# Kernel optimization log

Measured on AMD Instinct MI355X. Metric: run time of the kernel, lower is better.

## Reference

```python
import jax, jax.numpy as jnp
import numpy as np

D_MODEL = 1024
H = 16
D_K = D_MODEL // H
D_FF = 4096
EPS = 1e-6


def setup_inputs() -> dict:
    key = jax.random.key(0)
    ks = jax.random.split(key, 16)
    s = 1.0 / np.sqrt(D_MODEL)
    sf = 1.0 / np.sqrt(D_FF)
    inp = {
        'x': jax.random.normal(ks[0], (4, 2048, D_MODEL), dtype=jnp.float32),
        'wq': jax.random.uniform(ks[1], (D_MODEL, D_MODEL), minval=-s, maxval=s),
        'bq': jax.random.uniform(ks[2], (D_MODEL,), minval=-s, maxval=s),
        'wk': jax.random.uniform(ks[3], (D_MODEL, D_MODEL), minval=-s, maxval=s),
        'bk': jax.random.uniform(ks[4], (D_MODEL,), minval=-s, maxval=s),
        'wv': jax.random.uniform(ks[5], (D_MODEL, D_MODEL), minval=-s, maxval=s),
        'bv': jax.random.uniform(ks[6], (D_MODEL,), minval=-s, maxval=s),
        'wo': jax.random.uniform(ks[7], (D_MODEL, D_MODEL), minval=-s, maxval=s),
        'bo': jax.random.uniform(ks[8], (D_MODEL,), minval=-s, maxval=s),
        'w1': jax.random.uniform(ks[9], (D_MODEL, D_FF), minval=-s, maxval=s),
        'b1': jax.random.uniform(ks[10], (D_FF,), minval=-s, maxval=s),
        'w2': jax.random.uniform(ks[11], (D_FF, D_MODEL), minval=-sf, maxval=sf),
        'b2': jax.random.uniform(ks[12], (D_MODEL,), minval=-sf, maxval=sf),
        'alpha1': jnp.ones((1,), jnp.float32),
        'bias1': jnp.zeros((1,), jnp.float32),
        'alpha2': jnp.ones((1,), jnp.float32),
        'bias2': jnp.zeros((1,), jnp.float32),
    }
    return inp


def _layer_norm(x, alpha, bias):
    # torch: alpha*(x-mean)/(std+eps)+bias with unbiased std (ddof=1), eps on std
    m = jnp.mean(x, axis=-1, keepdims=True)
    s = jnp.std(x, axis=-1, keepdims=True, ddof=1)
    return alpha * (x - m) / (s + EPS) + bias


def _mha(x, wq, bq, wk, bk, wv, bv, wo, bo):
    B, S, _ = x.shape
    q = (x @ wq + bq).reshape(B, S, H, D_K).transpose(0, 2, 1, 3)
    k = (x @ wk + bk).reshape(B, S, H, D_K).transpose(0, 2, 1, 3)
    v = (x @ wv + bv).reshape(B, S, H, D_K).transpose(0, 2, 1, 3)
    scores = jnp.einsum('bhqd,bhkd->bhqk', q, k) / np.sqrt(D_K)
    attn = jax.nn.softmax(scores, axis=-1)
    out = jnp.einsum('bhqk,bhkd->bhqd', attn, v)
    out = out.transpose(0, 2, 1, 3).reshape(B, S, D_MODEL)
    return out @ wo + bo


def reference(x, wq, bq, wk, bk, wv, bv, wo, bo, w1, b1, w2, b2,
              alpha1, bias1, alpha2, bias2):
    # Residual 1: x + MHA(LN(x))
    h = x + _mha(_layer_norm(x, alpha1, bias1), wq, bq, wk, bk, wv, bv, wo, bo)
    # Residual 2: h + FFN(LN(h)); FFN = W2 relu(W1 z + b1) + b2
    z = _layer_norm(h, alpha2, bias2)
    ffn = jax.nn.relu(z @ w1 + b1) @ w2 + b2
    return h + ffn
```

## Files before the change

kernel.cpp:

```cpp
#include <hip/hip_runtime.h>
#include <hip/hip_bf16.h>
#include <cstdint>
#include <cstddef>

typedef __bf16 bf16;
typedef __bf16 bf16x4 __attribute__((ext_vector_type(4)));
typedef __bf16 bf16x8 __attribute__((ext_vector_type(8)));
typedef float f32x4 __attribute__((ext_vector_type(4)));

#define QK_SCALE 0.1803368801111204f

#define AS1 __attribute__((address_space(1)))
#define AS3 __attribute__((address_space(3)))

__device__ __forceinline__ void gload_lds16(const void* g, void* l) {
  __builtin_amdgcn_global_load_lds((AS1 void*)g, (AS3 void*)l, 16, 0, 0);
}

__device__ __forceinline__ float b2f(unsigned short u) {
  union { unsigned int i; float f; } v; v.i = (unsigned int)u << 16; return v.f;
}

__global__ __launch_bounds__(256)
void transpose_cvt(const float* __restrict__ in, bf16* __restrict__ out,
                   int K, int N) {
  __shared__ float t[32][33];
  const int tx = threadIdx.x, ty = threadIdx.y;
  const int n0 = blockIdx.x * 32, k0 = blockIdx.y * 32;
#pragma unroll
  for (int j = ty; j < 32; j += 8)
    t[j][tx] = in[(size_t)(k0 + j) * N + n0 + tx];
  __syncthreads();
#pragma unroll
  for (int j = ty; j < 32; j += 8)
    out[(size_t)(n0 + j) * K + k0 + tx] = (bf16)t[tx][j];
}

__global__ __launch_bounds__(256)
void transpose_cvt4(const float* __restrict__ wq, const float* __restrict__ wk,
                    const float* __restrict__ wv, const float* __restrict__ wo,
                    bf16* __restrict__ wqkvT, bf16* __restrict__ woT) {
  __shared__ float t[32][33];
  const int tx = threadIdx.x, ty = threadIdx.y, z = blockIdx.z;
  const float* in = (z == 0) ? wq : (z == 1) ? wk : (z == 2) ? wv : wo;
  bf16* out = (z < 3) ? wqkvT + (size_t)z * 1024 * 1024 : woT;
  const float sc = (z == 0) ? QK_SCALE : 1.0f;
  const int n0 = blockIdx.x * 32, k0 = blockIdx.y * 32;
#pragma unroll
  for (int j = ty; j < 32; j += 8)
    t[j][tx] = in[(size_t)(k0 + j) * 1024 + n0 + tx] * sc;
  __syncthreads();
#pragma unroll
  for (int j = ty; j < 32; j += 8)
    out[(size_t)(n0 + j) * 1024 + k0 + tx] = (bf16)t[tx][j];
}

__global__ __launch_bounds__(256)
void concat_bias(const float* __restrict__ bq, const float* __restrict__ bk,
                 const float* __restrict__ bv, float* __restrict__ o) {
  int i = blockIdx.x * 256 + threadIdx.x;
  if (i < 1024) o[i] = bq[i] * QK_SCALE;
  else if (i < 2048) o[i] = bk[i - 1024];
  else o[i] = bv[i - 2048];
}

__global__ __launch_bounds__(256)
void ln_kernel(const float* __restrict__ x, bf16* __restrict__ y,
               const float* __restrict__ alpha_p, const float* __restrict__ beta_p) {
  const int row = blockIdx.x;
  const float4 v = ((const float4*)(x + (size_t)row * 1024))[threadIdx.x];
  float s = v.x + v.y + v.z + v.w;
  float ss = v.x * v.x + v.y * v.y + v.z * v.z + v.w * v.w;
#pragma unroll
  for (int m = 1; m < 64; m <<= 1) {
    s += __shfl_xor(s, m);
    ss += __shfl_xor(ss, m);
  }
  __shared__ float red[8];
  const int wave = threadIdx.x >> 6, lane = threadIdx.x & 63;
  if (lane == 0) { red[wave] = s; red[4 + wave] = ss; }
  __syncthreads();
  s = red[0] + red[1] + red[2] + red[3];
  ss = red[4] + red[5] + red[6] + red[7];
  const float mean = s * (1.0f / 1024.0f);
  const float var = fmaxf(ss - 1024.0f * mean * mean, 0.0f) * (1.0f / 1023.0f);
  const float k = alpha_p[0] / (sqrtf(var) + 1e-6f);
  const float beta = beta_p[0];
  union { bf16 b[4]; uint2 u; } pk;
  pk.b[0] = (bf16)((v.x - mean) * k + beta);
  pk.b[1] = (bf16)((v.y - mean) * k + beta);
  pk.b[2] = (bf16)((v.z - mean) * k + beta);
  pk.b[3] = (bf16)((v.w - mean) * k + beta);
  ((uint2*)(y + (size_t)row * 1024))[threadIdx.x] = pk.u;
}

template <typename OutT, bool RELU, bool RESID>
__global__ __launch_bounds__(256)
void gemm_bt(const bf16* __restrict__ A, const bf16* __restrict__ Bt,
             const float* __restrict__ bias, const float* __restrict__ resid,
             OutT* __restrict__ C, int M, int N, int K) {
  __shared__ __align__(16) bf16 As[2][128 * 32];
  __shared__ __align__(16) bf16 Bs[2][128 * 32];
  const int tid = threadIdx.x;
  const int wave = tid >> 6, lane = tid & 63;
  const int l16 = lane & 15, lq = lane >> 4;
  const int nwg = gridDim.x * gridDim.y;
  const int id = blockIdx.y * gridDim.x + blockIdx.x;
  const int w = (id & 7) * (nwg >> 3) + (id >> 3);
  const int bm = (w / gridDim.y) * 128, bn = (w % gridDim.y) * 128;
  const int wr = wave >> 1, wc = wave & 1;

  const int tmp = (lane * 16) ^ (((lane >> 3) & 7) << 4);
  const int srow = tmp >> 6, sseg = (tmp >> 4) & 3;
  const bf16* Ab = A + (size_t)bm * K + sseg * 8;
  const bf16* Bb = Bt + (size_t)bn * K + sseg * 8;

  auto STAGE = [&](int k0, int buf) {
#pragma unroll
    for (int i = 0; i < 2; i++) {
      const int chunk = wave * 2 + i;
      const int r = chunk * 16 + srow;
      gload_lds16(Ab + (size_t)r * K + k0, (char*)As[buf] + chunk * 1024);
      gload_lds16(Bb + (size_t)r * K + k0, (char*)Bs[buf] + chunk * 1024);
    }
  };
  auto swz = [&](int row) -> int {
    return (row >> 1) * 128 + (((((row & 1) << 2) | lq) ^ ((row >> 1) & 7)) << 4);
  };

  STAGE(0, 0);
  __syncthreads();

  f32x4 acc[4][4] = {};
  const int nk = K >> 5;
  for (int t = 0; t < nk; t++) {
    const int cur = t & 1;
    if (t + 1 < nk) STAGE((t + 1) << 5, cur ^ 1);
    bf16x8 a[4], b[4];
#pragma unroll
    for (int m = 0; m < 4; m++)
      a[m] = *(const bf16x8*)((const char*)As[cur] + swz(wr * 64 + m * 16 + l16));
#pragma unroll
    for (int n = 0; n < 4; n++)
      b[n] = *(const bf16x8*)((const char*)Bs[cur] + swz(wc * 64 + n * 16 + l16));
#pragma unroll
    for (int m = 0; m < 4; m++)
#pragma unroll
      for (int n = 0; n < 4; n++)
        acc[m][n] = __builtin_amdgcn_mfma_f32_16x16x32_bf16(a[m], b[n], acc[m][n], 0, 0, 0);
    __syncthreads();
  }
#pragma unroll
  for (int m = 0; m < 4; m++) {
    const int row0 = bm + wr * 64 + m * 16 + lq * 4;
#pragma unroll
    for (int n = 0; n < 4; n++) {
      const int col = bn + wc * 64 + n * 16 + l16;
      const float bv = bias[col];
#pragma unroll
      for (int j = 0; j < 4; j++) {
        float v = acc[m][n][j] + bv;
        if (RELU) v = fmaxf(v, 0.0f);
        if (RESID) v += resid[(size_t)(row0 + j) * N + col];
        C[(size_t)(row0 + j) * N + col] = (OutT)v;
      }
    }
  }
}

template <typename OutT, bool RELU, bool BIAS>
__global__ __launch_bounds__(512, 2)
void gemm_v4(const bf16* __restrict__ A, const bf16* __restrict__ Bt,
             const float* __restrict__ bias, OutT* __restrict__ C,
             int lda, int ldb, int ldc, int K,
             int azs, int bzs, size_t czs) {
  __shared__ __align__(16) char lds[4 * 32768];
  const int tid = threadIdx.x;
  const int wave = tid >> 6, lane = tid & 63;
  const int l16 = lane & 15, lq = lane >> 4;
  const int wr = wave >> 2, wc = wave & 3;
  const int nwg = gridDim.x * gridDim.y;
  const int id = blockIdx.y * gridDim.x + blockIdx.x;
  const int w = (id & 7) * (nwg >> 3) + (id >> 3);
  const int bm = (w / gridDim.y) * 256, bn = (w % gridDim.y) * 256;

  A  += (size_t)blockIdx.z * azs;
  Bt += (size_t)blockIdx.z * bzs;
  C  += (size_t)blockIdx.z * czs;

  const int p = lane >> 3, jj = (lane & 7) ^ p;
  const int lrow = p * 2 + (jj >> 2), lseg = jj & 3;
  const bf16* Abase = A + (size_t)bm * lda + lseg * 8;
  const bf16* Bbase = Bt + (size_t)bn * ldb + lseg * 8;

  auto STAGEQ = [&](int t, int qq) {
    const int k0 = t << 5;
    const int grow = (qq & 1) * 128 + wave * 16 + lrow;
    const void* src = (qq < 2) ? (const void*)(Abase + (size_t)grow * lda + k0)
                               : (const void*)(Bbase + (size_t)grow * ldb + k0);
    gload_lds16(src, lds + (t & 3) * 32768 + qq * 8192 + wave * 1024);
  };
  auto swz = [&](int row) -> int {
    return (row >> 1) * 128 + (((((row & 1) << 2) | lq) ^ ((row >> 1) & 7)) << 4);
  };

  const int nk = K >> 5;
#pragma unroll
  for (int tt = 0; tt < 3; tt++)
#pragma unroll
    for (int qq = 0; qq < 4; qq++) STAGEQ(tt, qq);

  f32x4 acc[8][4] = {};
  for (int t = 0; t < nk; t++) {
    const char* buf = lds + (t & 3) * 32768;
    if (t + 2 < nk)      asm volatile("s_waitcnt vmcnt(8)" ::: "memory");
    else if (t + 1 < nk) asm volatile("s_waitcnt vmcnt(4)" ::: "memory");
    else                 asm volatile("s_waitcnt vmcnt(0)" ::: "memory");
    __builtin_amdgcn_s_barrier();
    __builtin_amdgcn_sched_barrier(0);
    if (t + 3 < nk) { STAGEQ(t + 3, 0); STAGEQ(t + 3, 1); }
    bf16x8 a0[4], b0[4], a1[4];
#pragma unroll
    for (int i = 0; i < 4; i++)
      a0[i] = *(const bf16x8*)(buf + swz(wr * 128 + i * 16 + l16));
#pragma unroll
    for (int n = 0; n < 4; n++)
      b0[n] = *(const bf16x8*)(buf + 16384 + swz(wc * 64 + n * 16 + l16));
    if (t + 3 < nk) { STAGEQ(t + 3, 2); STAGEQ(t + 3, 3); }
#pragma unroll
    for (int i = 0; i < 4; i++)
      a1[i] = *(const bf16x8*)(buf + swz(wr * 128 + 64 + i * 16 + l16));
    __builtin_amdgcn_sched_barrier(0);
    __builtin_amdgcn_s_setprio(1);
#pragma unroll
    for (int i = 0; i < 4; i++)
#pragma unroll
      for (int n = 0; n < 4; n++)
        acc[i][n] = __builtin_amdgcn_mfma_f32_16x16x32_bf16(a0[i], b0[n], acc[i][n], 0, 0, 0);
    __builtin_amdgcn_s_setprio(0);
    __builtin_amdgcn_sched_barrier(0);
    __builtin_amdgcn_s_setprio(1);
#pragma unroll
    for (int i = 0; i < 4; i++)
#pragma unroll
      for (int n = 0; n < 4; n++)
        acc[4 + i][n] = __builtin_amdgcn_mfma_f32_16x16x32_bf16(a1[i], b0[n], acc[4 + i][n], 0, 0, 0);
    __builtin_amdgcn_s_setprio(0);
  }
#pragma unroll
  for (int m = 0; m < 8; m++) {
    const int row0 = bm + wr * 128 + m * 16 + lq * 4;
#pragma unroll
    for (int n = 0; n < 4; n++) {
      const int col = bn + wc * 64 + n * 16 + l16;
      const float bv = BIAS ? bias[col] : 0.0f;
#pragma unroll
      for (int j = 0; j < 4; j++) {
        float v = acc[m][n][j] + bv;
        if (RELU) v = fmaxf(v, 0.0f);
        C[(size_t)(row0 + j) * ldc + col] = (OutT)v;
      }
    }
  }
}

__global__ __launch_bounds__(256)
void ffn2_reduce(const bf16* __restrict__ p0, const bf16* __restrict__ p1,
                 const float* __restrict__ b2, float* __restrict__ out) {
  const size_t i = (size_t)blockIdx.x * 256 + threadIdx.x;
  float4 h = ((const float4*)out)[i];
  const ushort4 a = ((const ushort4*)p0)[i];
  const ushort4 b = ((const ushort4*)p1)[i];
  const float4 bb = ((const float4*)b2)[i & 255];
  h.x += b2f(a.x) + b2f(b.x) + bb.x;
  h.y += b2f(a.y) + b2f(b.y) + bb.y;
  h.z += b2f(a.z) + b2f(b.z) + bb.z;
  h.w += b2f(a.w) + b2f(b.w) + bb.w;
  ((float4*)out)[i] = h;
}

__global__ __launch_bounds__(256)
void vt_prep(const bf16* __restrict__ qkv, bf16* __restrict__ Vt) {
  __shared__ __align__(16) bf16 Vl[64 * 64];
  const int tid = threadIdx.x;
  const int sblk = blockIdx.x, bh = blockIdx.y, b = bh >> 4, h = bh & 15;
  const size_t srow = (size_t)b * 2048 + sblk * 64;
  const bf16* src = qkv + srow * 3072 + 2048 + h * 64;
#pragma unroll
  for (int i = 0; i < 2; i++) {
    int c = i * 256 + tid;
    int s = c >> 3, dseg = c & 7;
    int col = dseg ^ (s & 7) ^ (s >> 3);
    *(uint4*)((char*)Vl + s * 128 + col * 16) =
        *(const uint4*)(src + (size_t)s * 3072 + dseg * 8);
  }
  __syncthreads();
  bf16* dst = Vt + (size_t)bh * 64 * 2048 + sblk * 64;
#pragma unroll
  for (int i = 0; i < 2; i++) {
    int c = i * 256 + tid;
    int d = c >> 3, grp = c & 7;
    union { bf16 v[8]; uint4 u; } pk;
#pragma unroll
    for (int j = 0; j < 8; j++) {
      int pp = grp * 8 + j;
      int s = (pp & 32) | (((pp >> 2) & 1) << 4) | (((pp >> 3) & 3) << 2) | (pp & 3);
      int col = (d >> 3) ^ (s & 7) ^ (s >> 3);
      pk.v[j] = *(const bf16*)((char*)Vl + s * 128 + col * 16 + ((2 * d) & 15));
    }
    *(uint4*)(dst + (size_t)d * 2048 + grp * 8) = pk.u;
  }
}

__global__ __launch_bounds__(256, 2)
void attn_kernel(const bf16* __restrict__ qkv, const bf16* __restrict__ Vt,
                 bf16* __restrict__ out) {
  __shared__ __align__(16) bf16 smem[40960];
  bf16* Qs = smem;
  bf16* Ks = smem + 16384;
  bf16* Vs = smem + 28672;
  const int tid = threadIdx.x, wave = tid >> 6, lane = tid & 63;
  const int l16 = lane & 15, lq = lane >> 4;
  const int id = blockIdx.y * 8 + blockIdx.x;
  const int w = (id & 7) * 64 + (id >> 3);
  const int qblk = w & 7, bh = w >> 3;
  const int b = bh >> 4, h = bh & 15;
  const int q0 = qblk * 256;
  const size_t rowbase = (size_t)b * 2048;
  const bf16* Qg = qkv + (rowbase + q0) * 3072 + h * 64;
  const bf16* Kg = qkv + rowbase * 3072 + 1024 + h * 64;
  const bf16* Vg = Vt + (size_t)bh * 64 * 2048;

#pragma unroll
  for (int i = 0; i < 8; i++) {
    const int c = i * 256 + wave * 64;
    const int cl = c + lane;
    const int r = cl >> 3, seg = cl & 7;
    gload_lds16(Qg + (size_t)r * 3072 + (seg ^ (r & 7)) * 8, (char*)Qs + c * 16);
  }
  auto stageKV = [&](int kt, int buf) {
    const int kv0 = kt * 64;
#pragma unroll
    for (int i = 0; i < 2; i++) {
      const int c = i * 256 + wave * 64;
      const int cl = c + lane;
      const int r = cl >> 3, seg = cl & 7;
      gload_lds16(Kg + (size_t)(kv0 + r) * 3072 + (seg ^ (r & 7)) * 8,
                  (char*)Ks + buf * 8192 + c * 16);
      gload_lds16(Vg + (size_t)r * 2048 + kv0 + (seg ^ (r & 7)) * 8,
                  (char*)Vs + buf * 8192 + c * 16);
    }
  };
  stageKV(0, 0);
  stageKV(1, 1);

  asm volatile("s_waitcnt vmcnt(8)" ::: "memory");
  __builtin_amdgcn_s_barrier();
  bf16x8 qb[4][2];
#pragma unroll
  for (int g = 0; g < 4; g++)
#pragma unroll
    for (int H = 0; H < 2; H++) {
      const int row = wave * 64 + g * 16 + l16;
      const int col = (H * 64 + lq * 16) ^ ((row & 7) << 4);
      qb[g][H] = *(const bf16x8*)((const char*)Qs + row * 128 + col);
    }

  f32x4 oacc[4][4] = {};
  f32x4 lacc[4] = {};
  bf16x8 onesb;
#pragma unroll
  for (int j = 0; j < 8; j++) onesb[j] = (bf16)1.0f;

  for (int t = 0; t < 32; t++) {
    if (t < 31) asm volatile("s_waitcnt vmcnt(4)" ::: "memory");
    else        asm volatile("s_waitcnt vmcnt(0)" ::: "memory");
    __builtin_amdgcn_s_barrier();
    __builtin_amdgcn_sched_barrier(0);
    if (t + 2 < 32) stageKV(t + 2, (t + 2) % 3);
    const char* Kb = (const char*)Ks + (t % 3) * 8192;
    const char* Vb = (const char*)Vs + (t % 3) * 8192;

    bf16x8 ka[2][4];
#pragma unroll
    for (int H = 0; H < 2; H++)
#pragma unroll
      for (int m = 0; m < 4; m++) {
        const int row = m * 16 + l16;
        const int col = (H * 64 + lq * 16) ^ ((row & 7) << 4);
        ka[H][m] = *(const bf16x8*)(Kb + row * 128 + col);
      }
    bf16x8 vb[2][4];
#pragma unroll
    for (int H = 0; H < 2; H++)
#pragma unroll
      for (int nd = 0; nd < 4; nd++) {
        const int row = nd * 16 + l16;
        const int col = (H * 64 + lq * 16) ^ ((row & 7) << 4);
        vb[H][nd] = *(const bf16x8*)(Vb + row * 128 + col);
      }
#pragma unroll
    for (int g = 0; g < 4; g++) {
      f32x4 sc[4];
      __builtin_amdgcn_s_setprio(1);
#pragma unroll
      for (int m = 0; m < 4; m++) {
        f32x4 z = {};
        sc[m] = __builtin_amdgcn_mfma_f32_16x16x32_bf16(ka[0][m], qb[g][0], z, 0, 0, 0);
        sc[m] = __builtin_amdgcn_mfma_f32_16x16x32_bf16(ka[1][m], qb[g][1], sc[m], 0, 0, 0);
      }
      __builtin_amdgcn_s_setprio(0);
      bf16x8 pa0, pa1;
#pragma unroll
      for (int m = 0; m < 2; m++)
#pragma unroll
        for (int r = 0; r < 4; r++)
          pa0[m * 4 + r] = (bf16)__builtin_amdgcn_exp2f(sc[m][r]);
#pragma unroll
      for (int m = 0; m < 2; m++)
#pragma unroll
        for (int r = 0; r < 4; r++)
          pa1[m * 4 + r] = (bf16)__builtin_amdgcn_exp2f(sc[2 + m][r]);
      __builtin_amdgcn_s_setprio(1);
#pragma unroll
      for (int nd = 0; nd < 4; nd++) {
        oacc[g][nd] = __builtin_amdgcn_mfma_f32_16x16x32_bf16(pa0, vb[0][nd], oacc[g][nd], 0, 0, 0);
        oacc[g][nd] = __builtin_amdgcn_mfma_f32_16x16x32_bf16(pa1, vb[1][nd], oacc[g][nd], 0, 0, 0);
      }
      lacc[g] = __builtin_amdgcn_mfma_f32_16x16x32_bf16(pa0, onesb, lacc[g], 0, 0, 0);
      lacc[g] = __builtin_amdgcn_mfma_f32_16x16x32_bf16(pa1, onesb, lacc[g], 0, 0, 0);
      __builtin_amdgcn_s_setprio(0);
    }
  }
#pragma unroll
  for (int g = 0; g < 4; g++) {
#pragma unroll
    for (int r = 0; r < 4; r++) {
      const float inv = 1.0f / lacc[g][r];
      const size_t row = rowbase + q0 + wave * 64 + g * 16 + lq * 4 + r;
#pragma unroll
      for (int nd = 0; nd < 4; nd++)
        out[row * 1024 + h * 64 + nd * 16 + l16] = (bf16)(oacc[g][nd][r] * inv);
    }
  }
}

extern "C" void kernel_launch(void* const* d_in, const int* in_sizes, int n_in,
                              void* d_out, int out_size, void* d_ws, size_t ws_size,
                              hipStream_t stream) {
  const float* x      = (const float*)d_in[0];
  const float* wq     = (const float*)d_in[1];
  const float* bq     = (const float*)d_in[2];
  const float* wk     = (const float*)d_in[3];
  const float* bk     = (const float*)d_in[4];
  const float* wv     = (const float*)d_in[5];
  const float* bv     = (const float*)d_in[6];
  const float* wo     = (const float*)d_in[7];
  const float* bo     = (const float*)d_in[8];
  const float* w1     = (const float*)d_in[9];
  const float* b1     = (const float*)d_in[10];
  const float* w2     = (const float*)d_in[11];
  const float* b2     = (const float*)d_in[12];
  const float* alpha1 = (const float*)d_in[13];
  const float* bias1  = (const float*)d_in[14];
  const float* alpha2 = (const float*)d_in[15];
  const float* bias2  = (const float*)d_in[16];
  float* out = (float*)d_out;

  const size_t MB = 1024ull * 1024ull;
  char* ws = (char*)d_ws;
  bf16*  wqkvT = (bf16*)(ws);
  bf16*  woT   = (bf16*)(ws + 6 * MB);
  bf16*  w1T   = (bf16*)(ws + 8 * MB);
  bf16*  w2T   = (bf16*)(ws + 16 * MB);
  float* bqkv  = (float*)(ws + 24 * MB);
  bf16*  Z     = (bf16*)(ws + 24 * MB + 65536);
  bf16*  Vtb   = Z;
  bf16*  QKV   = (bf16*)(ws + 40 * MB + 65536);
  bf16*  AO    = (bf16*)(ws + 88 * MB + 65536);
  bf16*  FFN1  = QKV;
  bf16*  PART  = (bf16*)ws;
  const size_t PART1_OFF = (24 * MB + 65536) / 2;

  const dim3 tb(32, 8);
  transpose_cvt4<<<dim3(32, 32, 4), tb, 0, stream>>>(wq, wk, wv, wo, wqkvT, woT);
  transpose_cvt<<<dim3(128, 32), tb, 0, stream>>>(w1, w1T, 1024, 4096);
  transpose_cvt<<<dim3(32, 128), tb, 0, stream>>>(w2, w2T, 4096, 1024);
  concat_bias<<<12, 256, 0, stream>>>(bq, bk, bv, bqkv);

  ln_kernel<<<8192, 256, 0, stream>>>(x, Z, alpha1, bias1);
  gemm_v4<bf16, false, true><<<dim3(32, 12), 512, 0, stream>>>(
      Z, wqkvT, bqkv, QKV, 1024, 1024, 3072, 1024, 0, 0, 0);
  vt_prep<<<dim3(32, 64), 256, 0, stream>>>(QKV, Vtb);
  attn_kernel<<<dim3(8, 64), 256, 0, stream>>>(QKV, Vtb, AO);
  gemm_bt<float, false, true><<<dim3(64, 8), 256, 0, stream>>>(
      AO, woT, bo, x, out, 8192, 1024, 1024);
  ln_kernel<<<8192, 256, 0, stream>>>(out, Z, alpha2, bias2);
  gemm_v4<bf16, true, true><<<dim3(32, 16), 512, 0, stream>>>(
      Z, w1T, b1, FFN1, 1024, 1024, 4096, 1024, 0, 0, 0);
  gemm_v4<bf16, false, false><<<dim3(32, 4, 2), 512, 0, stream>>>(
      FFN1, w2T, nullptr, PART, 4096, 4096, 1024, 2048, 2048, 2048, PART1_OFF);
  ffn2_reduce<<<8192, 256, 0, stream>>>(PART, PART + PART1_OFF, b2, out);
}
```

Measured before the change: 349.7 us.

## Restructure GEMM main loop into two-phase ping-pong with prefetch distance two

Rewrites the bf16 GEMM k-loop schedule. Global-to-LDS prefetch distance drops from three tiles to two, and each iteration is split into two halves. Each half issues its LDS reads and a portion of the next loads, then runs its MFMA block, with extra barriers and lgkmcnt waits between the halves. The aim is to interleave memory issue with MFMA work more evenly across waves, in exchange for more barriers per iteration and less latency hiding from the shorter prefetch.

```diff
diff --git a/kernel.cpp b/kernel.cpp
--- a/kernel.cpp
+++ b/kernel.cpp
@@ -193,43 +193,40 @@
   const bf16* Abase = A + (size_t)bm * lda + lseg * 8;
   const bf16* Bbase = Bt + (size_t)bn * ldb + lseg * 8;
 
-  auto STAGEQ = [&](int t, int qq) {
+  auto STAGEH = [&](int t, int half) {
     const int k0 = t << 5;
-    const int grow = (qq & 1) * 128 + wave * 16 + lrow;
-    const void* src = (qq < 2) ? (const void*)(Abase + (size_t)grow * lda + k0)
-                               : (const void*)(Bbase + (size_t)grow * ldb + k0);
-    gload_lds16(src, lds + (t & 3) * 32768 + qq * 8192 + wave * 1024);
+    const int grow = (half & 1) * 128 + wave * 16 + lrow;
+    const void* src = (half < 2) ? (const void*)(Abase + (size_t)grow * lda + k0)
+                                 : (const void*)(Bbase + (size_t)grow * ldb + k0);
+    gload_lds16(src, lds + (t & 3) * 32768 + (half >> 1) * 16384 +
+                         (half & 1) * 8192 + wave * 1024);
   };
   auto swz = [&](int row) -> int {
     return (row >> 1) * 128 + (((((row & 1) << 2) | lq) ^ ((row >> 1) & 7)) << 4);
   };
 
-  const int nk = K >> 5;
-#pragma unroll
-  for (int tt = 0; tt < 3; tt++)
-#pragma unroll
-    for (int qq = 0; qq < 4; qq++) STAGEQ(tt, qq);
+  const int nkt = K >> 5;
+#pragma unroll
+  for (int hh = 0; hh < 4; hh++) STAGEH(0, hh);
+#pragma unroll
+  for (int hh = 0; hh < 4; hh++) STAGEH(1, hh);
+  asm volatile("s_waitcnt vmcnt(4)" ::: "memory");
+  __builtin_amdgcn_s_barrier();
 
   f32x4 acc[8][4] = {};
-  for (int t = 0; t < nk; t++) {
-    const char* buf = lds + (t & 3) * 32768;
-    if (t + 2 < nk)      asm volatile("s_waitcnt vmcnt(8)" ::: "memory");
-    else if (t + 1 < nk) asm volatile("s_waitcnt vmcnt(4)" ::: "memory");
-    else                 asm volatile("s_waitcnt vmcnt(0)" ::: "memory");
+  for (int t = 0; t < nkt; t++) {
+    const char* bufA = lds + (t & 3) * 32768;
+    const char* bufB = bufA + 16384;
+    bf16x8 a0[4], b0[4], a1[4];
+#pragma unroll
+    for (int i = 0; i < 4; i++)
+      a0[i] = *(const bf16x8*)(bufA + swz(wr * 128 + i * 16 + l16));
+#pragma unroll
+    for (int n = 0; n < 4; n++)
+      b0[n] = *(const bf16x8*)(bufB + swz(wc * 64 + n * 16 + l16));
+    if (t + 2 < nkt) { STAGEH(t + 2, 0); STAGEH(t + 2, 2); }
     __builtin_amdgcn_s_barrier();
-    __builtin_amdgcn_sched_barrier(0);
-    if (t + 3 < nk) { STAGEQ(t + 3, 0); STAGEQ(t + 3, 1); }
-    bf16x8 a0[4], b0[4], a1[4];
-#pragma unroll
-    for (int i = 0; i < 4; i++)
-      a0[i] = *(const bf16x8*)(buf + swz(wr * 128 + i * 16 + l16));
-#pragma unroll
-    for (int n = 0; n < 4; n++)
-      b0[n] = *(const bf16x8*)(buf + 16384 + swz(wc * 64 + n * 16 + l16));
-    if (t + 3 < nk) { STAGEQ(t + 3, 2); STAGEQ(t + 3, 3); }
-#pragma unroll
-    for (int i = 0; i < 4; i++)
-      a1[i] = *(const bf16x8*)(buf + swz(wr * 128 + 64 + i * 16 + l16));
+    asm volatile("s_waitcnt lgkmcnt(0)" ::: "memory");
     __builtin_amdgcn_sched_barrier(0);
     __builtin_amdgcn_s_setprio(1);
 #pragma unroll
@@ -238,6 +235,15 @@
       for (int n = 0; n < 4; n++)
         acc[i][n] = __builtin_amdgcn_mfma_f32_16x16x32_bf16(a0[i], b0[n], acc[i][n], 0, 0, 0);
     __builtin_amdgcn_s_setprio(0);
+    __builtin_amdgcn_s_barrier();
+#pragma unroll
+    for (int i = 0; i < 4; i++)
+      a1[i] = *(const bf16x8*)(bufA + swz(wr * 128 + 64 + i * 16 + l16));
+    if (t + 2 < nkt) { STAGEH(t + 2, 1); STAGEH(t + 2, 3); }
+    if (t + 2 < nkt) asm volatile("s_waitcnt vmcnt(4)" ::: "memory");
+    else             asm volatile("s_waitcnt vmcnt(0)" ::: "memory");
+    __builtin_amdgcn_s_barrier();
+    asm volatile("s_waitcnt lgkmcnt(0)" ::: "memory");
     __builtin_amdgcn_sched_barrier(0);
     __builtin_amdgcn_s_setprio(1);
 #pragma unroll
@@ -246,6 +252,7 @@
       for (int n = 0; n < 4; n++)
         acc[4 + i][n] = __builtin_amdgcn_mfma_f32_16x16x32_bf16(a1[i], b0[n], acc[4 + i][n], 0, 0, 0);
     __builtin_amdgcn_s_setprio(0);
+    __builtin_amdgcn_s_barrier();
   }
 #pragma unroll
   for (int m = 0; m < 8; m++) {
```

Measured after the change: 354.8 us. About the same (+1.5%).
